# Kernel optimization log

Measured on AMD Instinct MI355X. Metric: run time of the kernel, lower is better.

The kernel has to match this reference:

```python
import jax, jax.numpy as jnp
import numpy as np

DILATIONS = (1, 2, 4, 8)
K = 3  # kernel_size
B, H, W, C = 16, 128, 128, 64
HID = 256
OUT = 64  # == C, so residual path is taken


def _depthwise(x, w, dilation):
    # x: [B,H,W,C], w: [K,K,1,C] (HWIO depthwise kernel)
    pad = dilation * (K // 2)
    return jax.lax.conv_general_dilated(
        x, w,
        window_strides=(1, 1),
        padding=[(pad, pad), (pad, pad)],
        rhs_dilation=(dilation, dilation),
        dimension_numbers=('NHWC', 'HWIO', 'NHWC'),
        feature_group_count=C,
    )


def setup_inputs() -> dict:
    key = jax.random.key(0)
    k_x, k_cw, k_w1, k_b1, k_w2, k_b2 = jax.random.split(key, 6)
    in_feat = C * (1 + len(DILATIONS))  # 320
    x = jax.random.normal(k_x, (B, H, W, C), jnp.float32)
    # depthwise kernels, one [K,K,1,C] per dilation, stacked
    conv_w = jax.random.normal(k_cw, (len(DILATIONS), K, K, 1, C), jnp.float32) * (1.0 / np.sqrt(K * K).astype(np.float32))
    W1 = jax.random.normal(k_w1, (in_feat, HID), jnp.float32) * np.float32(1.0 / np.sqrt(in_feat))
    b1 = jax.random.normal(k_b1, (HID,), jnp.float32) * 0.01
    W2 = jax.random.normal(k_w2, (HID, OUT), jnp.float32) * np.float32(1.0 / np.sqrt(HID))
    b2 = jax.random.normal(k_b2, (OUT,), jnp.float32) * 0.01
    return {"x": x, "conv_w": conv_w, "W1": W1, "b1": b1, "W2": W2, "b2": b2}


def reference(x, conv_w, W1, b1, W2, b2):
    # 1) Perception: multiscale depthwise dilated convs (same-padding per dilation)
    perceptions = [_depthwise(x, conv_w[i], d) for i, d in enumerate(DILATIONS)]
    upd_in = jnp.concatenate([x] + perceptions, axis=-1)  # [B,H,W,5C]
    # 2) Update MLP: Linear -> Dropout(eval: identity) -> GELU(exact erf) -> Linear
    h = jax.nn.gelu(upd_in @ W1 + b1, approximate=False)  # [B,H,W,HID]
    delta = h @ W2 + b2  # [B,H,W,OUT]
    # 3) out_channels == channels and (eval mode or fire_rate==1.0): plain residual
    return x + delta
```

## Files before the change

kernel.cpp:

```cpp
#include <hip/hip_runtime.h>
#include <hip/hip_fp16.h>
#include <cstdint>

#define B_   16
#define H_   128
#define W_   128
#define C_   64
#define HID_ 256
#define XELEMS (B_ * H_ * W_ * C_)

typedef _Float16 __attribute__((ext_vector_type(2))) half2v;
typedef _Float16 __attribute__((ext_vector_type(8))) half8v;
typedef __attribute__((ext_vector_type(4))) float f32x4;
typedef unsigned short ushort_t;

#define W1S_OFF 0
#define W2S_OFF 81920
#define CWH_OFF 98304
#define XH_OFF  100608
#define FEAT_OFF (XH_OFF + XELEMS)
#define FEAT_HALVES (4096ull * 16384ull)
#define WS_NEED_FULL (2ull * (FEAT_OFF + FEAT_HALVES))

__device__ __forceinline__ int hs(int row, int col) {
  return row * 256 + (((col >> 3) ^ (row & 7)) << 3) + (col & 7);
}

__device__ __forceinline__ float fast_gelu(float h) {
  float u = h * fmaf(h * h, 0.10293921f, 2.30211813f);
  float e = exp2f(-u);
  return h * __builtin_amdgcn_rcpf(1.0f + e);
}

__device__ __forceinline__ uint32_t fast_gelu_pk(float h0, float h1) {
  half2v h = __builtin_bit_cast(half2v, __builtin_amdgcn_cvt_pkrtz(h0, h1));
  const half2v c1 = {(_Float16)0.10293921f, (_Float16)0.10293921f};
  const half2v c0 = {(_Float16)2.30211813f, (_Float16)2.30211813f};
  half2v u = h * (c0 + h * h * c1);
  __half2 e = h2exp2(__hneg2(__builtin_bit_cast(__half2, u)));
  const __half2 one = __half2{(__half)1.0f, (__half)1.0f};
  __half2 s = h2rcp(__hadd2(one, e));
  __half2 g = __hmul2(__builtin_bit_cast(__half2, h), s);
  return __builtin_bit_cast(uint32_t, g);
}

__device__ __forceinline__ void stage16(const _Float16* g, const ushort_t* l) {
  __builtin_amdgcn_global_load_lds(
      (const __attribute__((address_space(1))) void*)g,
      (__attribute__((address_space(3))) void*)l, 16, 0, 0);
}

__device__ __forceinline__ half2v bch(uint32_t u) {
  return __builtin_bit_cast(half2v, u);
}

__global__ void prep_kernel(const float* __restrict__ x,
                            const float* __restrict__ W1,
                            const float* __restrict__ W2,
                            const float* __restrict__ cw,
                            _Float16* __restrict__ wsb) {
  if (blockIdx.x < 393) {
    int t = blockIdx.x * 256 + threadIdx.x;
    if (t < 81920) {
      int j = t & 7, lane = (t >> 3) & 63, n16 = (t >> 9) & 15, ks = t >> 13;
      int k = ks * 32 + (lane >> 4) * 8 + j;
      int n = n16 * 16 + (lane & 15);
      wsb[W1S_OFF + t] = (_Float16)W1[k * 256 + n];
    } else if (t < 98304) {
      int t2 = t - 81920;
      int j = t2 & 7, lane = (t2 >> 3) & 63, n16 = (t2 >> 9) & 3, ks = t2 >> 11;
      int k = ks * 32 + (lane >> 4) * 8 + j;
      int n = n16 * 16 + (lane & 15);
      wsb[W2S_OFF + t2] = (_Float16)W2[k * 64 + n];
    } else if (t < 98304 + 2304) {
      int t3 = t - 98304;
      wsb[CWH_OFF + t3] = (_Float16)cw[t3];
    }
  } else {
    int i = ((blockIdx.x - 393) * 256 + threadIdx.x) * 8;
    const float4 a = *(const float4*)&x[i];
    const float4 b = *(const float4*)&x[i + 4];
    half8v o = {(_Float16)a.x, (_Float16)a.y, (_Float16)a.z, (_Float16)a.w,
                (_Float16)b.x, (_Float16)b.y, (_Float16)b.z, (_Float16)b.w};
    *(half8v*)&wsb[XH_OFF + i] = o;
  }
}

__device__ void conv_boundary(const _Float16* __restrict__ xhb,
                              const _Float16* __restrict__ cwh,
                              _Float16* __restrict__ ft,
                              int tid, int tileX, int tileY, int dil, int dd) {
  const int quad = tid & 15;
  const int p0   = tid >> 4;
  const int ksq  = quad >> 3;
  const int c32  = (quad & 7) * 4;

  half2v w01[9], w23[9];
#pragma unroll
  for (int t = 0; t < 9; ++t) {
    uint2 wr = *(const uint2*)&cwh[(dd * 9 + t) * C_ + quad * 4];
    w01[t] = bch(wr.x);
    w23[t] = bch(wr.y);
  }
#pragma unroll
  for (int i = 0; i < 4; ++i) {
    const int p  = i * 16 + p0;
    const int y0 = tileY + (p >> 3), x0 = tileX + (p & 7);
    half2v a01 = {0, 0}, a23 = {0, 0};
#pragma unroll
    for (int ky = 0; ky < 3; ++ky) {
      const int yy = y0 + (ky - 1) * dil;
#pragma unroll
      for (int kx = 0; kx < 3; ++kx) {
        const int xx = x0 + (kx - 1) * dil;
        uint2 vv = {0u, 0u};
        if ((unsigned)yy < (unsigned)H_ && (unsigned)xx < (unsigned)W_)
          vv = *(const uint2*)&xhb[(yy * W_ + xx) * C_ + quad * 4];
        const int t = ky * 3 + kx;
        a01 += bch(vv.x) * w01[t];
        a23 += bch(vv.y) * w23[t];
      }
    }
    uint2 pk;
    pk.x = __builtin_bit_cast(uint32_t, a01);
    pk.y = __builtin_bit_cast(uint32_t, a23);
    *(uint2*)&ft[(dd * 2 + ksq) * 2048 + p * 32 + c32] = pk;
  }
}

__global__ __launch_bounds__(256, 4)
void conv_all_kernel(const _Float16* __restrict__ xh,
                     const _Float16* __restrict__ cwh,
                     _Float16* __restrict__ feat) {
  __shared__ __align__(16) ushort_t lds[16 * 1024];

  const int tid   = threadIdx.x;
  const int tileX = blockIdx.x * 8;
  const int tileY = blockIdx.y * 8;
  const int batch = blockIdx.z >> 2;
  const int dd    = blockIdx.z & 3;
  const int dil   = 1 << dd;

  const _Float16* xhb = xh + (size_t)batch * (H_ * W_ * C_);
  _Float16* ft =
      feat + ((size_t)((batch * 16 + blockIdx.y) * 16 + blockIdx.x)) * 16384;

  const bool interior = (tileX >= 8) && (tileX <= W_ - 16) &&
                        (tileY >= 8) && (tileY <= H_ - 16);

  if (dd == 3) {
    const int c8 = tid & 7;
    const int p0 = tid >> 3;
    const int ksq = c8 >> 2;
    const int cof = (c8 & 3) * 8;

    uint4 wv4[9];
#pragma unroll
    for (int t = 0; t < 9; ++t)
      wv4[t] = *(const uint4*)&cwh[(3 * 9 + t) * C_ + c8 * 8];

    uint4 v[2][9];
#pragma unroll
    for (int i = 0; i < 2; ++i) {
      const int p  = i * 32 + p0;
      const int y0 = tileY + (p >> 3), x0 = tileX + (p & 7);
      if (interior) {
#pragma unroll
        for (int ky = 0; ky < 3; ++ky)
#pragma unroll
          for (int kx = 0; kx < 3; ++kx)
            v[i][ky * 3 + kx] = *(const uint4*)
                &xhb[((y0 + (ky - 1) * 8) * W_ + x0 + (kx - 1) * 8) * C_ +
                     c8 * 8];
      } else {
#pragma unroll
        for (int ky = 0; ky < 3; ++ky)
#pragma unroll
          for (int kx = 0; kx < 3; ++kx) {
            const int yy = y0 + (ky - 1) * 8;
            const int xx = x0 + (kx - 1) * 8;
            uint4 vv = {0u, 0u, 0u, 0u};
            if ((unsigned)yy < (unsigned)H_ && (unsigned)xx < (unsigned)W_)
              vv = *(const uint4*)&xhb[(yy * W_ + xx) * C_ + c8 * 8];
            v[i][ky * 3 + kx] = vv;
          }
      }
    }
#pragma unroll
    for (int i = 0; i < 2; ++i)
#pragma unroll
      for (int t = 0; t < 9; ++t)
        asm volatile("" : "+v"(v[i][t].x), "+v"(v[i][t].y),
                          "+v"(v[i][t].z), "+v"(v[i][t].w));

#pragma unroll
    for (int i = 0; i < 2; ++i) {
      const int p = i * 32 + p0;
      half2v a0 = {0, 0}, a1 = {0, 0}, a2 = {0, 0}, a3 = {0, 0};
#pragma unroll
      for (int t = 0; t < 9; ++t) {
        a0 += bch(v[i][t].x) * bch(wv4[t].x);
        a1 += bch(v[i][t].y) * bch(wv4[t].y);
        a2 += bch(v[i][t].z) * bch(wv4[t].z);
        a3 += bch(v[i][t].w) * bch(wv4[t].w);
      }
      uint4 pk;
      pk.x = __builtin_bit_cast(uint32_t, a0);
      pk.y = __builtin_bit_cast(uint32_t, a1);
      pk.z = __builtin_bit_cast(uint32_t, a2);
      pk.w = __builtin_bit_cast(uint32_t, a3);
      *(uint4*)&ft[(3 * 2 + ksq) * 2048 + p * 32 + cof] = pk;
    }
    return;
  }

  if (!interior) {
    conv_boundary(xhb, cwh, ft, tid, tileX, tileY, dil, dd);
    return;
  }

  const int lane = tid & 63;
  const int wv   = tid >> 6;
  const int quad = tid & 15;
  const int p0   = tid >> 4;
  const int ksq  = quad >> 3;
  const int c32  = (quad & 7) * 4;
  const int R    = 8 + 2 * dil;

  {
    const int x0 = tileX - dil, y0 = tileY - dil;
    for (int s = wv; s < 2 * R; s += 4) {
      const int row = s >> 1, half = s & 1;
      const _Float16* g =
          &xhb[((y0 + row) * W_ + x0 + half * 8 + (lane >> 3)) * C_ +
               (lane & 7) * 8];
      stage16(g, &lds[row * 1024 + half * 512]);
    }
  }

  half2v w01[9], w23[9];
#pragma unroll
  for (int t = 0; t < 9; ++t) {
    uint2 wr = *(const uint2*)&cwh[(dd * 9 + t) * C_ + quad * 4];
    w01[t] = bch(wr.x);
    w23[t] = bch(wr.y);
  }

  __syncthreads();

#pragma unroll
  for (int i = 0; i < 4; ++i) {
    const int p  = i * 16 + p0;
    const int py = p >> 3, px = p & 7;
    uint2 tv[9];
#pragma unroll
    for (int ky = 0; ky < 3; ++ky)
#pragma unroll
      for (int kx = 0; kx < 3; ++kx)
        tv[ky * 3 + kx] = *(const uint2*)
            &lds[(py + ky * dil) * 1024 + (px + kx * dil) * 64 + quad * 4];
    half2v a01 = {0, 0}, a23 = {0, 0};
#pragma unroll
    for (int t = 0; t < 9; ++t) {
      a01 += bch(tv[t].x) * w01[t];
      a23 += bch(tv[t].y) * w23[t];
    }
    uint2 pk;
    pk.x = __builtin_bit_cast(uint32_t, a01);
    pk.y = __builtin_bit_cast(uint32_t, a23);
    *(uint2*)&ft[(dd * 2 + ksq) * 2048 + p * 32 + c32] = pk;
  }
}

__global__ __launch_bounds__(256, 4)
void mlp_kernel(const _Float16* __restrict__ xh,
                const _Float16* __restrict__ feat,
                const float* __restrict__ b1,
                const float* __restrict__ b2,
                const _Float16* __restrict__ w1s,
                const _Float16* __restrict__ w2s,
                float* __restrict__ out) {
  __shared__ __align__(16) ushort_t smem[64 * 256];

  const int tid   = threadIdx.x;
  const int tileX = blockIdx.x * 8;
  const int tileY = blockIdx.y * 8;
  const int batch = blockIdx.z;
  const _Float16* xhb = xh + (size_t)batch * (H_ * W_ * C_);
  const _Float16* ftb =
      feat + ((size_t)((batch * 16 + blockIdx.y) * 16 + blockIdx.x)) * 16384;

  const int lane = tid & 63;
  const int wv   = tid >> 6;
  const int lr   = lane & 15;
  const int lg   = lane >> 4;
  const int n0   = wv * 64;

  const half8v* w1v = (const half8v*)w1s;

  half8v xf[4][2];
#pragma unroll
  for (int pi = 0; pi < 4; ++pi) {
    const int p  = pi * 16 + lr;
    const int gp = (tileY + (p >> 3)) * W_ + tileX + (p & 7);
#pragma unroll
    for (int ks = 0; ks < 2; ++ks)
      xf[pi][ks] = *(const half8v*)&xhb[gp * C_ + ks * 32 + lg * 8];
  }

  {
    const _Float16* src0 = &ftb[(wv * 16 + lr) * 32 + lg * 8];
#pragma unroll
    for (int s = 0; s < 8; ++s)
      stage16(src0 + s * 2048, &smem[(s * 4 + wv) * 512]);
  }

  f32x4 acc[4][4];
#pragma unroll
  for (int hi = 0; hi < 4; ++hi)
#pragma unroll
    for (int pi = 0; pi < 4; ++pi) acc[hi][pi] = 0;

#pragma unroll
  for (int ks = 0; ks < 2; ++ks) {
    half8v wf[4];
#pragma unroll
    for (int hi = 0; hi < 4; ++hi)
      wf[hi] = w1v[(ks * 16 + wv * 4 + hi) * 64 + lane];
#pragma unroll
    for (int hi = 0; hi < 4; ++hi)
#pragma unroll
      for (int pi = 0; pi < 4; ++pi)
        acc[hi][pi] = __builtin_amdgcn_mfma_f32_16x16x32_f16(
            wf[hi], xf[pi][ks], acc[hi][pi], 0, 0, 0);
  }

  __syncthreads();

#define LOAD_W(WB, S)                                                         \
  _Pragma("unroll") for (int hi = 0; hi < 4; ++hi)                            \
      WB[hi] = w1v[((S) * 16 + wv * 4 + hi) * 64 + lane];
#define LOAD_F(FB, S)                                                         \
  _Pragma("unroll") for (int pi = 0; pi < 4; ++pi)                            \
      FB[pi] = *(const half8v*)&smem[(((S) - 2) * 4 + pi) * 512 + lane * 8];
#define MFMA16(WB, FB)                                                        \
  _Pragma("unroll") for (int hi = 0; hi < 4; ++hi)                            \
      _Pragma("unroll") for (int pi = 0; pi < 4; ++pi)                        \
      acc[hi][pi] = __builtin_amdgcn_mfma_f32_16x16x32_f16(                   \
          WB[hi], FB[pi], acc[hi][pi], 0, 0, 0);

  {
    half8v wfA[4], wfB[4], fA[4];
    LOAD_W(wfA, 2);
    LOAD_F(fA, 2); LOAD_W(wfB, 3); MFMA16(wfA, fA);
    LOAD_F(fA, 3); LOAD_W(wfA, 4); MFMA16(wfB, fA);
    LOAD_F(fA, 4); LOAD_W(wfB, 5); MFMA16(wfA, fA);
    LOAD_F(fA, 5); LOAD_W(wfA, 6); MFMA16(wfB, fA);
    LOAD_F(fA, 6); LOAD_W(wfB, 7); MFMA16(wfA, fA);
    LOAD_F(fA, 7); LOAD_W(wfA, 8); MFMA16(wfB, fA);
    LOAD_F(fA, 8); LOAD_W(wfB, 9); MFMA16(wfA, fA);
    LOAD_F(fA, 9);                 MFMA16(wfB, fA);
  }

  float4 bias1[4];
#pragma unroll
  for (int hi = 0; hi < 4; ++hi)
    bias1[hi] = *(const float4*)&b1[n0 + hi * 16 + lg * 4];

  __syncthreads();

#pragma unroll
  for (int hi = 0; hi < 4; ++hi) {
#pragma unroll
    for (int pi = 0; pi < 4; ++pi) {
      uint2 pk;
      pk.x = fast_gelu_pk(acc[hi][pi][0] + bias1[hi][0],
                          acc[hi][pi][1] + bias1[hi][1]);
      pk.y = fast_gelu_pk(acc[hi][pi][2] + bias1[hi][2],
                          acc[hi][pi][3] + bias1[hi][3]);
      *(uint2*)&smem[hs(pi * 16 + lr, n0 + hi * 16 + lg * 4)] = pk;
    }
  }
  __syncthreads();

  const int m0 = wv * 16;
  f32x4 acc2[4];
#pragma unroll
  for (int ni = 0; ni < 4; ++ni) acc2[ni] = 0;

  const half8v* w2v = (const half8v*)w2s;
#pragma unroll 2
  for (int ks = 0; ks < 8; ++ks) {
    half8v a2 = *(const half8v*)&smem[hs(m0 + lr, ks * 32 + lg * 8)];
#pragma unroll
    for (int ni = 0; ni < 4; ++ni) {
      half8v bfr = w2v[(ks * 4 + ni) * 64 + lane];
      acc2[ni] = __builtin_amdgcn_mfma_f32_16x16x32_f16(a2, bfr, acc2[ni],
                                                        0, 0, 0);
    }
  }

#pragma unroll
  for (int ni = 0; ni < 4; ++ni) {
    const int col  = ni * 16 + lr;
    const float bias = b2[col];
#pragma unroll
    for (int q = 0; q < 4; ++q) {
      const int row = m0 + lg * 4 + q;
      const int py = row >> 3, px = row & 7;
      const size_t idx =
          ((size_t)(batch * H_ + tileY + py) * W_ + (tileX + px)) * C_ + col;
      out[idx] = (float)xh[idx] + acc2[ni][q] + bias;
    }
  }
#undef LOAD_W
#undef LOAD_F
#undef MFMA16
}

template <bool BOUND>
__device__ __forceinline__ void conv_phase_f32(const float* __restrict__ xb,
                                               const _Float16* __restrict__ cwh,
                                               ushort_t* __restrict__ feat,
                                               int tid, int tileX, int tileY) {
  const int quad = tid & 15;
  const int p0   = tid >> 4;
#pragma unroll
  for (int dd = 0; dd < 4; ++dd) {
    const int dil = 1 << dd;
    half2v w01[9], w23[9];
#pragma unroll
    for (int t = 0; t < 9; ++t) {
      uint2 wr = *(const uint2*)&cwh[(dd * 9 + t) * C_ + quad * 4];
      w01[t] = bch(wr.x);
      w23[t] = bch(wr.y);
    }
#pragma unroll
    for (int i = 0; i < 4; ++i) {
      const int p  = i * 16 + p0;
      const int y0 = tileY + (p >> 3), x0 = tileX + (p & 7);
      half2v a01 = {0, 0}, a23 = {0, 0};
#pragma unroll
      for (int ky = 0; ky < 3; ++ky) {
        const int yy = y0 + (ky - 1) * dil;
        if (BOUND && (unsigned)yy >= (unsigned)H_) continue;
#pragma unroll
        for (int kx = 0; kx < 3; ++kx) {
          const int xx = x0 + (kx - 1) * dil;
          if (BOUND && (unsigned)xx >= (unsigned)W_) continue;
          const int t = ky * 3 + kx;
          const float4 xv = *(const float4*)&xb[(yy * W_ + xx) * C_ + quad * 4];
          half2v xl = {(_Float16)xv.x, (_Float16)xv.y};
          half2v xh2 = {(_Float16)xv.z, (_Float16)xv.w};
          a01 += xl * w01[t];
          a23 += xh2 * w23[t];
        }
      }
      uint2 pk;
      pk.x = __builtin_bit_cast(uint32_t, a01);
      pk.y = __builtin_bit_cast(uint32_t, a23);
      *(uint2*)&feat[hs(p, dd * 64 + quad * 4)] = pk;
    }
  }
}

__global__ __launch_bounds__(256, 4)
void nca_fused_fp32(const float* __restrict__ x,
                    const _Float16* __restrict__ cwh,
                    const float* __restrict__ b1,
                    const float* __restrict__ b2,
                    const _Float16* __restrict__ w1s,
                    const _Float16* __restrict__ w2s,
                    float* __restrict__ out) {
  __shared__ __align__(16) ushort_t smem[64 * 256];

  const int tid   = threadIdx.x;
  const int tileX = blockIdx.x * 8;
  const int tileY = blockIdx.y * 8;
  const int batch = blockIdx.z;
  const float* xb = x + (size_t)batch * (H_ * W_ * C_);

  const int lane = tid & 63;
  const int wv   = tid >> 6;
  const int lr   = lane & 15;
  const int lg   = lane >> 4;
  const int n0   = wv * 64;

  half8v xf[4][2];
#pragma unroll
  for (int pi = 0; pi < 4; ++pi) {
    const int p  = pi * 16 + lr;
    const int gp = (tileY + (p >> 3)) * W_ + tileX + (p & 7);
#pragma unroll
    for (int ks = 0; ks < 2; ++ks) {
      const float* bp = &xb[gp * C_ + ks * 32 + lg * 8];
      float4 u = *(const float4*)bp, v = *(const float4*)(bp + 4);
      half8v s = {(_Float16)u.x, (_Float16)u.y, (_Float16)u.z, (_Float16)u.w,
                  (_Float16)v.x, (_Float16)v.y, (_Float16)v.z, (_Float16)v.w};
      xf[pi][ks] = s;
    }
  }

  const bool interior = (tileX >= 8) && (tileX <= W_ - 16) &&
                        (tileY >= 8) && (tileY <= H_ - 16);
  if (interior)
    conv_phase_f32<false>(xb, cwh, smem, tid, tileX, tileY);
  else
    conv_phase_f32<true>(xb, cwh, smem, tid, tileX, tileY);
  __syncthreads();

  f32x4 acc[4][4];
#pragma unroll
  for (int hi = 0; hi < 4; ++hi)
#pragma unroll
    for (int pi = 0; pi < 4; ++pi) acc[hi][pi] = 0;

  const half8v* w1v = (const half8v*)w1s;
#pragma unroll
  for (int ks = 0; ks < 2; ++ks) {
    half8v wf[4];
#pragma unroll
    for (int hi = 0; hi < 4; ++hi)
      wf[hi] = w1v[(ks * 16 + wv * 4 + hi) * 64 + lane];
#pragma unroll
    for (int hi = 0; hi < 4; ++hi)
#pragma unroll
      for (int pi = 0; pi < 4; ++pi)
        acc[hi][pi] = __builtin_amdgcn_mfma_f32_16x16x32_f16(
            wf[hi], xf[pi][ks], acc[hi][pi], 0, 0, 0);
  }
  for (int ks = 2; ks < 10; ++ks) {
    half8v ff[4], wf[4];
#pragma unroll
    for (int pi = 0; pi < 4; ++pi)
      ff[pi] = *(const half8v*)&smem[hs(pi * 16 + lr, (ks - 2) * 32 + lg * 8)];
#pragma unroll
    for (int hi = 0; hi < 4; ++hi)
      wf[hi] = w1v[(ks * 16 + wv * 4 + hi) * 64 + lane];
#pragma unroll
    for (int hi = 0; hi < 4; ++hi)
#pragma unroll
      for (int pi = 0; pi < 4; ++pi)
        acc[hi][pi] = __builtin_amdgcn_mfma_f32_16x16x32_f16(
            wf[hi], ff[pi], acc[hi][pi], 0, 0, 0);
  }

  float4 bias1[4];
#pragma unroll
  for (int hi = 0; hi < 4; ++hi)
    bias1[hi] = *(const float4*)&b1[n0 + hi * 16 + lg * 4];

  __syncthreads();

#pragma unroll
  for (int hi = 0; hi < 4; ++hi) {
#pragma unroll
    for (int pi = 0; pi < 4; ++pi) {
      _Float16 g[4];
#pragma unroll
      for (int q = 0; q < 4; ++q)
        g[q] = (_Float16)fast_gelu(acc[hi][pi][q] + bias1[hi][q]);
      half2v g01 = {g[0], g[1]}, g23 = {g[2], g[3]};
      uint2 pk;
      pk.x = __builtin_bit_cast(uint32_t, g01);
      pk.y = __builtin_bit_cast(uint32_t, g23);
      *(uint2*)&smem[hs(pi * 16 + lr, n0 + hi * 16 + lg * 4)] = pk;
    }
  }
  __syncthreads();

  const int m0 = wv * 16;
  f32x4 acc2[4];
#pragma unroll
  for (int ni = 0; ni < 4; ++ni) acc2[ni] = 0;

  const half8v* w2v = (const half8v*)w2s;
  for (int ks = 0; ks < 8; ++ks) {
    half8v a2 = *(const half8v*)&smem[hs(m0 + lr, ks * 32 + lg * 8)];
#pragma unroll
    for (int ni = 0; ni < 4; ++ni) {
      half8v bfr = w2v[(ks * 4 + ni) * 64 + lane];
      acc2[ni] = __builtin_amdgcn_mfma_f32_16x16x32_f16(a2, bfr, acc2[ni],
                                                        0, 0, 0);
    }
  }

#pragma unroll
  for (int ni = 0; ni < 4; ++ni) {
    const int col  = ni * 16 + lr;
    const float bias = b2[col];
#pragma unroll
    for (int q = 0; q < 4; ++q) {
      const int row = m0 + lg * 4 + q;
      const int py = row >> 3, px = row & 7;
      const size_t idx =
          ((size_t)(batch * H_ + tileY + py) * W_ + (tileX + px)) * C_ + col;
      out[idx] = x[idx] + acc2[ni][q] + bias;
    }
  }
}

extern "C" void kernel_launch(void* const* d_in, const int* in_sizes, int n_in,
                              void* d_out, int out_size, void* d_ws,
                              size_t ws_size, hipStream_t stream) {
  const float* x  = (const float*)d_in[0];
  const float* cw = (const float*)d_in[1];
  const float* W1 = (const float*)d_in[2];
  const float* b1 = (const float*)d_in[3];
  const float* W2 = (const float*)d_in[4];
  const float* b2 = (const float*)d_in[5];
  float* out = (float*)d_out;

  _Float16* wsb  = (_Float16*)d_ws;
  _Float16* w1s  = wsb + W1S_OFF;
  _Float16* w2s  = wsb + W2S_OFF;
  _Float16* cwh  = wsb + CWH_OFF;
  _Float16* xh   = wsb + XH_OFF;
  _Float16* feat = wsb + FEAT_OFF;

  if (ws_size >= (size_t)WS_NEED_FULL) {
    prep_kernel<<<393 + XELEMS / 8 / 256, 256, 0, stream>>>(x, W1, W2, cw, wsb);
    dim3 cgrid(W_ / 8, H_ / 8, B_ * 4);
    conv_all_kernel<<<cgrid, 256, 0, stream>>>(xh, cwh, feat);
    dim3 mgrid(W_ / 8, H_ / 8, B_);
    mlp_kernel<<<mgrid, 256, 0, stream>>>(xh, feat, b1, b2, w1s, w2s, out);
  } else {
    prep_kernel<<<393, 256, 0, stream>>>(x, W1, W2, cw, wsb);
    dim3 grid(W_ / 8, H_ / 8, B_);
    nca_fused_fp32<<<grid, 256, 0, stream>>>(x, cwh, b1, b2, w1s, w2s, out);
  }
}
```

Before: 181.4 us.

## Split MLP kernel across 8 waves with unified LDS staging of x and features

The MLP kernel now runs with 512 threads (8 waves) per 64-pixel tile. Each wave computes 32 hidden units instead of 64, which halves the accumulator registers per wave, and in the second GEMM each wave computes two of the four output column blocks. The x inputs are now staged through LDS together with the precomputed features (40 fragments of 512 halves) instead of being loaded straight into registers. The aim is more waves in flight to hide latency, at the cost of a larger LDS footprint and more loads of W1 and W2 across waves.

```diff
diff --git a/kernel.cpp b/kernel.cpp
--- a/kernel.cpp
+++ b/kernel.cpp
@@ -272,7 +272,7 @@
   }
 }
 
-__global__ __launch_bounds__(256, 4)
+__global__ __launch_bounds__(512, 5)
 void mlp_kernel(const _Float16* __restrict__ xh,
                 const _Float16* __restrict__ feat,
                 const float* __restrict__ b1,
@@ -280,7 +280,7 @@
                 const _Float16* __restrict__ w1s,
                 const _Float16* __restrict__ w2s,
                 float* __restrict__ out) {
-  __shared__ __align__(16) ushort_t smem[64 * 256];
+  __shared__ __align__(16) ushort_t smem[40 * 512];
 
   const int tid   = threadIdx.x;
   const int tileX = blockIdx.x * 8;
@@ -291,86 +291,70 @@
       feat + ((size_t)((batch * 16 + blockIdx.y) * 16 + blockIdx.x)) * 16384;
 
   const int lane = tid & 63;
-  const int wv   = tid >> 6;
+  const int w8   = tid >> 6;
   const int lr   = lane & 15;
   const int lg   = lane >> 4;
-  const int n0   = wv * 64;
+  const int n0   = w8 * 32;
 
   const half8v* w1v = (const half8v*)w1s;
 
-  half8v xf[4][2];
-#pragma unroll
-  for (int pi = 0; pi < 4; ++pi) {
+  for (int r = w8; r < 40; r += 8) {
+    const int ks = r >> 2, pi = r & 3;
     const int p  = pi * 16 + lr;
-    const int gp = (tileY + (p >> 3)) * W_ + tileX + (p & 7);
-#pragma unroll
-    for (int ks = 0; ks < 2; ++ks)
-      xf[pi][ks] = *(const half8v*)&xhb[gp * C_ + ks * 32 + lg * 8];
-  }
-
-  {
-    const _Float16* src0 = &ftb[(wv * 16 + lr) * 32 + lg * 8];
-#pragma unroll
-    for (int s = 0; s < 8; ++s)
-      stage16(src0 + s * 2048, &smem[(s * 4 + wv) * 512]);
-  }
-
-  f32x4 acc[4][4];
-#pragma unroll
-  for (int hi = 0; hi < 4; ++hi)
+    const _Float16* g;
+    if (ks < 2) {
+      const int gp = (tileY + (p >> 3)) * W_ + tileX + (p & 7);
+      g = &xhb[gp * C_ + ks * 32 + lg * 8];
+    } else {
+      g = &ftb[(ks - 2) * 2048 + p * 32 + lg * 8];
+    }
+    stage16(g, &smem[r * 512]);
+  }
+
+  float4 bias1[2];
+#pragma unroll
+  for (int hi = 0; hi < 2; ++hi)
+    bias1[hi] = *(const float4*)&b1[n0 + hi * 16 + lg * 4];
+
+  f32x4 acc[2][4];
+#pragma unroll
+  for (int hi = 0; hi < 2; ++hi)
 #pragma unroll
     for (int pi = 0; pi < 4; ++pi) acc[hi][pi] = 0;
 
-#pragma unroll
-  for (int ks = 0; ks < 2; ++ks) {
-    half8v wf[4];
-#pragma unroll
-    for (int hi = 0; hi < 4; ++hi)
-      wf[hi] = w1v[(ks * 16 + wv * 4 + hi) * 64 + lane];
-#pragma unroll
-    for (int hi = 0; hi < 4; ++hi)
-#pragma unroll
-      for (int pi = 0; pi < 4; ++pi)
-        acc[hi][pi] = __builtin_amdgcn_mfma_f32_16x16x32_f16(
-            wf[hi], xf[pi][ks], acc[hi][pi], 0, 0, 0);
-  }
-
   __syncthreads();
 
 #define LOAD_W(WB, S)                                                         \
-  _Pragma("unroll") for (int hi = 0; hi < 4; ++hi)                            \
-      WB[hi] = w1v[((S) * 16 + wv * 4 + hi) * 64 + lane];
+  _Pragma("unroll") for (int hi = 0; hi < 2; ++hi)                            \
+      WB[hi] = w1v[((S) * 16 + w8 * 2 + hi) * 64 + lane];
 #define LOAD_F(FB, S)                                                         \
   _Pragma("unroll") for (int pi = 0; pi < 4; ++pi)                            \
-      FB[pi] = *(const half8v*)&smem[(((S) - 2) * 4 + pi) * 512 + lane * 8];
-#define MFMA16(WB, FB)                                                        \
-  _Pragma("unroll") for (int hi = 0; hi < 4; ++hi)                            \
+      FB[pi] = *(const half8v*)&smem[((S) * 4 + pi) * 512 + lane * 8];
+#define MFMA8(WB, FB)                                                         \
+  _Pragma("unroll") for (int hi = 0; hi < 2; ++hi)                            \
       _Pragma("unroll") for (int pi = 0; pi < 4; ++pi)                        \
       acc[hi][pi] = __builtin_amdgcn_mfma_f32_16x16x32_f16(                   \
           WB[hi], FB[pi], acc[hi][pi], 0, 0, 0);
 
   {
-    half8v wfA[4], wfB[4], fA[4];
-    LOAD_W(wfA, 2);
-    LOAD_F(fA, 2); LOAD_W(wfB, 3); MFMA16(wfA, fA);
-    LOAD_F(fA, 3); LOAD_W(wfA, 4); MFMA16(wfB, fA);
-    LOAD_F(fA, 4); LOAD_W(wfB, 5); MFMA16(wfA, fA);
-    LOAD_F(fA, 5); LOAD_W(wfA, 6); MFMA16(wfB, fA);
-    LOAD_F(fA, 6); LOAD_W(wfB, 7); MFMA16(wfA, fA);
-    LOAD_F(fA, 7); LOAD_W(wfA, 8); MFMA16(wfB, fA);
-    LOAD_F(fA, 8); LOAD_W(wfB, 9); MFMA16(wfA, fA);
-    LOAD_F(fA, 9);                 MFMA16(wfB, fA);
-  }
-
-  float4 bias1[4];
-#pragma unroll
-  for (int hi = 0; hi < 4; ++hi)
-    bias1[hi] = *(const float4*)&b1[n0 + hi * 16 + lg * 4];
+    half8v wfA[2], wfB[2], fA[4];
+    LOAD_W(wfA, 0);
+    LOAD_F(fA, 0); LOAD_W(wfB, 1); MFMA8(wfA, fA);
+    LOAD_F(fA, 1); LOAD_W(wfA, 2); MFMA8(wfB, fA);
+    LOAD_F(fA, 2); LOAD_W(wfB, 3); MFMA8(wfA, fA);
+    LOAD_F(fA, 3); LOAD_W(wfA, 4); MFMA8(wfB, fA);
+    LOAD_F(fA, 4); LOAD_W(wfB, 5); MFMA8(wfA, fA);
+    LOAD_F(fA, 5); LOAD_W(wfA, 6); MFMA8(wfB, fA);
+    LOAD_F(fA, 6); LOAD_W(wfB, 7); MFMA8(wfA, fA);
+    LOAD_F(fA, 7); LOAD_W(wfA, 8); MFMA8(wfB, fA);
+    LOAD_F(fA, 8); LOAD_W(wfB, 9); MFMA8(wfA, fA);
+    LOAD_F(fA, 9);                 MFMA8(wfB, fA);
+  }
 
   __syncthreads();
 
 #pragma unroll
-  for (int hi = 0; hi < 4; ++hi) {
+  for (int hi = 0; hi < 2; ++hi) {
 #pragma unroll
     for (int pi = 0; pi < 4; ++pi) {
       uint2 pk;
@@ -383,26 +367,27 @@
   }
   __syncthreads();
 
-  const int m0 = wv * 16;
-  f32x4 acc2[4];
-#pragma unroll
-  for (int ni = 0; ni < 4; ++ni) acc2[ni] = 0;
+  const int m0    = (w8 & 3) * 16;
+  const int nbase = (w8 >> 2) * 2;
+  f32x4 acc2[2];
+#pragma unroll
+  for (int oi = 0; oi < 2; ++oi) acc2[oi] = 0;
 
   const half8v* w2v = (const half8v*)w2s;
 #pragma unroll 2
   for (int ks = 0; ks < 8; ++ks) {
     half8v a2 = *(const half8v*)&smem[hs(m0 + lr, ks * 32 + lg * 8)];
 #pragma unroll
-    for (int ni = 0; ni < 4; ++ni) {
-      half8v bfr = w2v[(ks * 4 + ni) * 64 + lane];
-      acc2[ni] = __builtin_amdgcn_mfma_f32_16x16x32_f16(a2, bfr, acc2[ni],
+    for (int oi = 0; oi < 2; ++oi) {
+      half8v bfr = w2v[(ks * 4 + nbase + oi) * 64 + lane];
+      acc2[oi] = __builtin_amdgcn_mfma_f32_16x16x32_f16(a2, bfr, acc2[oi],
                                                         0, 0, 0);
     }
   }
 
 #pragma unroll
-  for (int ni = 0; ni < 4; ++ni) {
-    const int col  = ni * 16 + lr;
+  for (int oi = 0; oi < 2; ++oi) {
+    const int col  = (nbase + oi) * 16 + lr;
     const float bias = b2[col];
 #pragma unroll
     for (int q = 0; q < 4; ++q) {
@@ -410,12 +395,12 @@
       const int py = row >> 3, px = row & 7;
       const size_t idx =
           ((size_t)(batch * H_ + tileY + py) * W_ + (tileX + px)) * C_ + col;
-      out[idx] = (float)xh[idx] + acc2[ni][q] + bias;
+      out[idx] = (float)xh[idx] + acc2[oi][q] + bias;
     }
   }
 #undef LOAD_W
 #undef LOAD_F
-#undef MFMA16
+#undef MFMA8
 }
 
 template <bool BOUND>
@@ -623,7 +608,7 @@
     dim3 cgrid(W_ / 8, H_ / 8, B_ * 4);
     conv_all_kernel<<<cgrid, 256, 0, stream>>>(xh, cwh, feat);
     dim3 mgrid(W_ / 8, H_ / 8, B_);
-    mlp_kernel<<<mgrid, 256, 0, stream>>>(xh, feat, b1, b2, w1s, w2s, out);
+    mlp_kernel<<<mgrid, 512, 0, stream>>>(xh, feat, b1, b2, w1s, w2s, out);
   } else {
     prep_kernel<<<393, 256, 0, stream>>>(x, W1, W2, cw, wsb);
     dim3 grid(W_ / 8, H_ / 8, B_);
```

Result: faster. 177.6 us (-2.1%).
